# Performance work log

Measured on AMD Instinct MI355X. Metric: run time of the kernel, lower is better.

## Reference

```python
import jax, jax.numpy as jnp
import numpy as np

D_MODEL = 512
NUM_HEADS = 8
D_FF = 2048
HEAD_DIM = D_MODEL // NUM_HEADS
EPS = 1e-8


def rmsnorm(x, scale):
    rms = jax.lax.rsqrt(jnp.mean(x * x, axis=-1, keepdims=True) + EPS)
    return scale * x * rms


def alibi_bias(seq_len, num_heads):
    # faithful to: 1.0 / (arange(1,H+1) * 2**arange(0,8)[:,None]).flatten()[:H]
    a = jnp.arange(1, num_heads + 1, dtype=jnp.float32)          # (H,)
    b = 2.0 ** jnp.arange(0, 8, dtype=jnp.float32)[:, None]       # (8,1)
    slopes = (1.0 / (a * b).reshape(-1))[:num_heads]               # (H,)
    pos = jnp.arange(seq_len)
    dist = jnp.abs(pos[:, None] - pos[None, :]).astype(jnp.float32)  # (S,S)
    return -slopes[:, None, None] * dist[None]                     # (H,S,S)


def setup_inputs() -> dict:
    key = jax.random.key(0)
    ks = jax.random.split(key, 12)
    s = 0.02
    return {
        "x": jax.random.normal(ks[0], (2, 2048, D_MODEL), dtype=jnp.float32),
        "norm1_scale": jnp.ones((D_MODEL,), jnp.float32),
        "norm2_scale": jnp.ones((D_MODEL,), jnp.float32),
        "in_proj_w": jax.random.normal(ks[1], (3 * D_MODEL, D_MODEL), jnp.float32) * s,
        "in_proj_b": jnp.zeros((3 * D_MODEL,), jnp.float32),
        "out_proj_w": jax.random.normal(ks[2], (D_MODEL, D_MODEL), jnp.float32) * s,
        "out_proj_b": jnp.zeros((D_MODEL,), jnp.float32),
        "w1": jax.random.normal(ks[3], (D_FF, D_MODEL), jnp.float32) * s,
        "b1": jnp.zeros((D_FF,), jnp.float32),
        "w2": jax.random.normal(ks[4], (D_MODEL, D_FF), jnp.float32) * s,
        "b2": jnp.zeros((D_MODEL,), jnp.float32),
    }


def reference(x, norm1_scale, norm2_scale, in_proj_w, in_proj_b,
              out_proj_w, out_proj_b, w1, b1, w2, b2):
    B, S, D = x.shape
    xn = rmsnorm(x, norm1_scale)
    qkv = xn @ in_proj_w.T + in_proj_b                      # (B,S,3D)
    q, k, v = jnp.split(qkv, 3, axis=-1)
    q = q.reshape(B, S, NUM_HEADS, HEAD_DIM)
    k = k.reshape(B, S, NUM_HEADS, HEAD_DIM)
    v = v.reshape(B, S, NUM_HEADS, HEAD_DIM)
    scale = 1.0 / jnp.sqrt(jnp.float32(HEAD_DIM))
    scores = jnp.einsum('bqhd,bkhd->bhqk', q, k) * scale    # (B,H,S,S)
    scores = scores + alibi_bias(S, NUM_HEADS)[None]
    attn = jax.nn.softmax(scores, axis=-1)
    ctx = jnp.einsum('bhqk,bkhd->bqhd', attn, v).reshape(B, S, D)
    attn_out = ctx @ out_proj_w.T + out_proj_b
    x = x + attn_out                                        # dropout is identity (eval)
    xn2 = rmsnorm(x, norm2_scale)
    h = jax.nn.gelu(xn2 @ w1.T + b1, approximate=False)
    mlp_out = h @ w2.T + b2
    return x + mlp_out
```

## Files before the change

kernel.cpp:

```cpp
#include <hip/hip_runtime.h>
#include <math.h>


typedef __bf16 bf16x8 __attribute__((ext_vector_type(8)));
typedef float  f32x4  __attribute__((ext_vector_type(4)));

#define TOKENS 4096
#define DMODEL 512
#define SEQ    2048
#define SPLITK 4
#define QSCALE 0.1803368801f

__device__ __forceinline__ void gl_lds16(const __bf16* g, __bf16* l) {
    __builtin_amdgcn_global_load_lds(
        (const __attribute__((address_space(1))) void*)g,
        (__attribute__((address_space(3))) void*)l, 16, 0, 0);
}

union PkU { unsigned u; __bf16 h[2]; };

__global__ void cvt_all(const float* __restrict__ w0, const float* __restrict__ w1,
                        const float* __restrict__ w2, const float* __restrict__ w3,
                        __bf16* __restrict__ d0, __bf16* __restrict__ d1,
                        __bf16* __restrict__ d2, __bf16* __restrict__ d3) {
    const int N0 = 1536 * 512, N1 = 512 * 512, N2 = 2048 * 512, N3 = 512 * 2048;
    int i4 = (blockIdx.x * 256 + threadIdx.x) * 4;
    const float* s; __bf16* d;
    if (i4 < N0)                   { s = w0 + i4;  d = d0 + i4; }
    else if ((i4 -= N0) < N1)      { s = w1 + i4;  d = d1 + i4; }
    else if ((i4 -= N1) < N2)      { s = w2 + i4;  d = d2 + i4; }
    else if ((i4 -= N2) < N3)      { s = w3 + i4;  d = d3 + i4; }
    else return;
    float4 v = *(const float4*)s;
    d[0] = (__bf16)v.x; d[1] = (__bf16)v.y; d[2] = (__bf16)v.z; d[3] = (__bf16)v.w;
}

__global__ void rmsnorm_kernel(const float* __restrict__ x, const float* __restrict__ scale,
                               __bf16* __restrict__ out) {
    int wave = threadIdx.x >> 6, lane = threadIdx.x & 63;
    int tok = blockIdx.x * 4 + wave;
    const float* row = x + (size_t)tok * DMODEL;
    float4 v0 = *(const float4*)&row[lane * 4];
    float4 v1 = *(const float4*)&row[256 + lane * 4];
    float ss = v0.x*v0.x + v0.y*v0.y + v0.z*v0.z + v0.w*v0.w
             + v1.x*v1.x + v1.y*v1.y + v1.z*v1.z + v1.w*v1.w;
    #pragma unroll
    for (int off = 1; off < 64; off <<= 1) ss += __shfl_xor(ss, off);
    float r = rsqrtf(ss * (1.0f / DMODEL) + 1e-8f);
    __bf16* o = out + (size_t)tok * DMODEL;
    o[lane*4 + 0] = (__bf16)(v0.x * r * scale[lane*4 + 0]);
    o[lane*4 + 1] = (__bf16)(v0.y * r * scale[lane*4 + 1]);
    o[lane*4 + 2] = (__bf16)(v0.z * r * scale[lane*4 + 2]);
    o[lane*4 + 3] = (__bf16)(v0.w * r * scale[lane*4 + 3]);
    o[256 + lane*4 + 0] = (__bf16)(v1.x * r * scale[256 + lane*4 + 0]);
    o[256 + lane*4 + 1] = (__bf16)(v1.y * r * scale[256 + lane*4 + 1]);
    o[256 + lane*4 + 2] = (__bf16)(v1.z * r * scale[256 + lane*4 + 2]);
    o[256 + lane*4 + 3] = (__bf16)(v1.w * r * scale[256 + lane*4 + 3]);
}

template <int EPI, int TM>
__global__ __launch_bounds__(256) void gemm_bt(
    const __bf16* __restrict__ A, const __bf16* __restrict__ W,
    const float* __restrict__ bias, const float* __restrict__ res,
    float* __restrict__ Cf, __bf16* __restrict__ Cb,
    __bf16* __restrict__ qb, __bf16* __restrict__ kb, __bf16* __restrict__ vtb,
    int M, int N, int K)
{
    constexpr int RI = TM / 32;
    __shared__ alignas(16) __bf16 As[2][TM * 32];
    __shared__ alignas(16) __bf16 Bs[2][128 * 32];
    const int tid = threadIdx.x;
    const int bm = blockIdx.x * TM;
    const int bn = blockIdx.y * 128;
    const int wave = tid >> 6, lane = tid & 63;
    const int wm = (wave & 1) * (TM / 2), wn = (wave >> 1) * 64;
    const int lrow = lane & 15;
    const int kq = (lane >> 4) * 8;

    f32x4 acc[RI][4] = {};

    for (int k0 = 0; k0 < K; k0 += 64) {
        __syncthreads();
        #pragma unroll
        for (int i = 0; i < TM / 32; i++) {
            int tt = i * 256 + tid;
            int kh = tt / (TM * 4), rem = tt % (TM * 4);
            int mrow = rem >> 2, c8 = rem & 3;
            gl_lds16(&A[(size_t)(bm + mrow) * K + k0 + kh * 32 + c8 * 8],
                     (__bf16*)As + tt * 8);
        }
        #pragma unroll
        for (int i = 0; i < 4; i++) {
            int tt = i * 256 + tid;
            int kh = tt >> 9, rem = tt & 511;
            int nrow = rem >> 2, c8 = rem & 3;
            gl_lds16(&W[(size_t)(bn + nrow) * K + k0 + kh * 32 + c8 * 8],
                     (__bf16*)Bs + tt * 8);
        }
        __syncthreads();
        #pragma unroll
        for (int kh = 0; kh < 2; kh++) {
            bf16x8 af[RI], bfv[4];
            #pragma unroll
            for (int i = 0; i < RI; i++) af[i] = *(bf16x8*)&As[kh][(wm + i*16 + lrow)*32 + kq];
            #pragma unroll
            for (int j = 0; j < 4; j++) bfv[j] = *(bf16x8*)&Bs[kh][(wn + j*16 + lrow)*32 + kq];
            #pragma unroll
            for (int i = 0; i < RI; i++)
                #pragma unroll
                for (int j = 0; j < 4; j++)
                    acc[i][j] = __builtin_amdgcn_mfma_f32_16x16x32_bf16(af[i], bfv[j], acc[i][j], 0, 0, 0);
        }
    }

    const int crow0 = (lane >> 4) * 4;
    const int ccol = lane & 15;
    const int quad = lane >> 4;

    if (EPI == 4) {
        #pragma unroll
        for (int j = 0; j < 4; j++) {
            const int col = bn + wn + j * 16 + ccol;
            const float bv = bias[col];
            if (col < 512) {
                const int h = col >> 6, d = col & 63;
                #pragma unroll
                for (int i = 0; i < RI; i++) {
                    const int row0 = bm + wm + i * 16 + crow0;
                    const int b = row0 >> 11, s0 = row0 & 2047;
                    #pragma unroll
                    for (int r = 0; r < 4; r++)
                        qb[(((size_t)b*8 + h)*2048 + s0 + r)*64 + d] =
                            (__bf16)((acc[i][j][r] + bv) * QSCALE);
                }
            } else if (col < 1024) {
                const int h = (col - 512) >> 6, d = col & 63;
                #pragma unroll
                for (int i = 0; i < RI; i++) {
                    const int row0 = bm + wm + i * 16 + crow0;
                    const int b = row0 >> 11, s0 = row0 & 2047;
                    #pragma unroll
                    for (int r = 0; r < 4; r++)
                        kb[(((size_t)b*8 + h)*2048 + s0 + r)*64 + d] = (__bf16)(acc[i][j][r] + bv);
                }
            } else {
                const int h = (col - 1024) >> 6, d = col & 63;
                const int tok0 = bm + wm;
                const int b = tok0 >> 11, sbase = tok0 & 2047;
                unsigned* vrow = (unsigned*)vtb + (((size_t)b*8 + h)*64 + d) * 1024 + (sbase >> 1);
                #pragma unroll
                for (int r = 0; r < 4; r++) {
                    PkU pk;
                    pk.h[0] = (__bf16)(acc[0][j][r] + bv);
                    pk.h[1] = (__bf16)(acc[1][j][r] + bv);
                    vrow[quad * 4 + r] = pk.u;
                }
            }
        }
    } else {
        #pragma unroll
        for (int i = 0; i < RI; i++) {
            const int row0 = bm + wm + i * 16 + crow0;
            #pragma unroll
            for (int j = 0; j < 4; j++) {
                const int col = bn + wn + j * 16 + ccol;
                const float bv = bias[col];
                if (EPI == 1) {
                    #pragma unroll
                    for (int r = 0; r < 4; r++) {
                        const size_t idx = (size_t)(row0 + r) * N + col;
                        Cf[idx] = res[idx] + acc[i][j][r] + bv;
                    }
                } else {
                    #pragma unroll
                    for (int r = 0; r < 4; r++) {
                        float v = acc[i][j][r] + bv;
                        Cb[(size_t)(row0 + r) * N + col] =
                            (__bf16)(0.5f * v * (1.0f + erff(v * 0.70710678f)));
                    }
                }
            }
        }
    }
}

__global__ __launch_bounds__(256, 4) void attn_kernel(
    const __bf16* __restrict__ qb, const __bf16* __restrict__ kb,
    const __bf16* __restrict__ vtb,
    float* __restrict__ Opart, float* __restrict__ lpart)
{
    const int qt = blockIdx.x, bh = blockIdx.y, sp = blockIdx.z;
    const int h = bh & 7;
    const int tid = threadIdx.x, wave = tid >> 6, lane = tid & 63;
    const int lrow = lane & 15, quad = lane >> 4;

    __shared__ alignas(16) __bf16 Ks[2][64 * 32];
    __shared__ alignas(16) __bf16 Vt[2][64 * 32];
    __shared__ alignas(16) unsigned Pt4[4][2][32][20];

    const float slope2 = -1.44269504f / (float)(h + 1);
    const int qbase = qt * 128 + wave * 32;

    bf16x8 qf[2][2];
    #pragma unroll
    for (int rt = 0; rt < 2; rt++)
        #pragma unroll
        for (int dh = 0; dh < 2; dh++)
            qf[rt][dh] = *(const bf16x8*)&qb[((size_t)bh*2048 + qbase + rt*16 + lrow)*64 + dh*32 + quad*8];

    bf16x8 ones;
    #pragma unroll
    for (int j = 0; j < 8; j++) ones[j] = (__bf16)1.0f;

    f32x4 O[2][4] = {};
    f32x4 lacc[2] = {};

    for (int kt = sp * (32 / SPLITK); kt < (sp + 1) * (32 / SPLITK); kt++) {
        const int kbase = kt * 64;
        __syncthreads();
        {
            #pragma unroll
            for (int i = 0; i < 2; i++) {
                int tt = i * 256 + tid;
                int dh = tt >> 8, key = (tt & 255) >> 2, c8 = (tt & 3) * 8;
                gl_lds16(&kb[((size_t)bh*2048 + kbase + key)*64 + dh*32 + c8],
                         (__bf16*)Ks + tt * 8);
            }
            #pragma unroll
            for (int i = 0; i < 2; i++) {
                int tt = i * 256 + tid;
                int kh = tt >> 8, d = (tt & 255) >> 2, ck = (tt & 3) * 8;
                gl_lds16(&vtb[((size_t)bh*64 + d)*2048 + kbase + kh*32 + ck],
                         (__bf16*)Vt + tt * 8);
            }
        }
        __syncthreads();

        bf16x8 kf[4][2];
        #pragma unroll
        for (int j = 0; j < 4; j++)
            #pragma unroll
            for (int dh = 0; dh < 2; dh++)
                kf[j][dh] = *(bf16x8*)&Ks[dh][(j*16 + lrow)*32 + quad*8];

        #pragma unroll
        for (int rt = 0; rt < 2; rt++) {
            f32x4 Sc[4] = {};
            #pragma unroll
            for (int dh = 0; dh < 2; dh++)
                #pragma unroll
                for (int j = 0; j < 4; j++)
                    Sc[j] = __builtin_amdgcn_mfma_f32_16x16x32_bf16(qf[rt][dh], kf[j][dh], Sc[j], 0, 0, 0);

            const float dbase = (float)(qbase + rt*16 + quad*4 - kbase - lrow);
            #pragma unroll
            for (int r = 0; r < 4; r++) {
                const float d0 = dbase + (float)r;
                #pragma unroll
                for (int jp = 0; jp < 2; jp++) {
                    float v0 = fmaf(slope2, fabsf(d0 - (float)(jp*32)),      Sc[2*jp  ][r]);
                    float v1 = fmaf(slope2, fabsf(d0 - (float)(jp*32 + 16)), Sc[2*jp+1][r]);
                    PkU pk;
                    pk.h[0] = (__bf16)exp2f(v0);
                    pk.h[1] = (__bf16)exp2f(v1);
                    Pt4[wave][jp][rt*16 + quad*4 + r][lrow] = pk.u;
                }
            }
        }

        bf16x8 pf[2][2];
        #pragma unroll
        for (int rt = 0; rt < 2; rt++)
            #pragma unroll
            for (int kh = 0; kh < 2; kh++)
                pf[rt][kh] = *(bf16x8*)&Pt4[wave][kh][rt*16 + lrow][quad*4];

        #pragma unroll
        for (int rt = 0; rt < 2; rt++)
            #pragma unroll
            for (int kh = 0; kh < 2; kh++)
                lacc[rt] = __builtin_amdgcn_mfma_f32_16x16x32_bf16(pf[rt][kh], ones, lacc[rt], 0, 0, 0);

        #pragma unroll
        for (int dt = 0; dt < 4; dt++) {
            #pragma unroll
            for (int kh = 0; kh < 2; kh++) {
                bf16x8 vf = *(bf16x8*)&Vt[kh][(dt*16 + lrow)*32 + quad*8];
                #pragma unroll
                for (int rt = 0; rt < 2; rt++)
                    O[rt][dt] = __builtin_amdgcn_mfma_f32_16x16x32_bf16(pf[rt][kh], vf, O[rt][dt], 0, 0, 0);
            }
        }
    }

    #pragma unroll
    for (int rt = 0; rt < 2; rt++) {
        #pragma unroll
        for (int dt = 0; dt < 4; dt++)
            #pragma unroll
            for (int r = 0; r < 4; r++) {
                const int q = qbase + rt*16 + quad*4 + r;
                Opart[(((size_t)sp*16 + bh)*2048 + q)*64 + dt*16 + lrow] = O[rt][dt][r];
            }
        if (lrow == 0) {
            #pragma unroll
            for (int r = 0; r < 4; r++)
                lpart[((size_t)sp*16 + bh)*2048 + qbase + rt*16 + quad*4 + r] = lacc[rt][r];
        }
    }
}

__global__ void combine_kernel(const float* __restrict__ Opart, const float* __restrict__ lpart,
                               __bf16* __restrict__ ctx) {
    const int idx = blockIdx.x * 256 + threadIdx.x;
    const int d2 = idx & 31;
    const int q  = (idx >> 5) & 2047;
    const int bh = idx >> 16;
    float ox = 0.0f, oy = 0.0f, l = 0.0f;
    #pragma unroll
    for (int sp = 0; sp < SPLITK; sp++) {
        const float2 o = *(const float2*)&Opart[(((size_t)sp*16 + bh)*2048 + q)*64 + d2*2];
        ox += o.x; oy += o.y;
        l += lpart[((size_t)sp*16 + bh)*2048 + q];
    }
    const float inv = 1.0f / l;
    PkU pk;
    pk.h[0] = (__bf16)(ox * inv);
    pk.h[1] = (__bf16)(oy * inv);
    const int b = bh >> 3, h = bh & 7;
    *((unsigned*)ctx + (((size_t)b*2048 + q)*512 + h*64) / 2 + d2) = pk.u;
}

extern "C" void kernel_launch(void* const* d_in, const int* in_sizes, int n_in,
                              void* d_out, int out_size, void* d_ws, size_t ws_size,
                              hipStream_t stream) {
    const float* x    = (const float*)d_in[0];
    const float* n1s  = (const float*)d_in[1];
    const float* n2s  = (const float*)d_in[2];
    const float* wqkv = (const float*)d_in[3];
    const float* bqkv = (const float*)d_in[4];
    const float* wout = (const float*)d_in[5];
    const float* bout = (const float*)d_in[6];
    const float* w1   = (const float*)d_in[7];
    const float* b1   = (const float*)d_in[8];
    const float* w2   = (const float*)d_in[9];
    const float* b2   = (const float*)d_in[10];
    float* out = (float*)d_out;

    char* ws = (char*)d_ws;
    __bf16* xn1    = (__bf16*)ws; ws += (size_t)TOKENS * DMODEL * 2;
    __bf16* qbuf   = (__bf16*)ws; ws += (size_t)TOKENS * DMODEL * 2;
    __bf16* kbuf   = (__bf16*)ws; ws += (size_t)TOKENS * DMODEL * 2;
    __bf16* vtbuf  = (__bf16*)ws; ws += (size_t)TOKENS * DMODEL * 2;
    __bf16* wqkv_b = (__bf16*)ws; ws += (size_t)1536 * DMODEL * 2;
    __bf16* wout_b = (__bf16*)ws; ws += (size_t)DMODEL * DMODEL * 2;
    __bf16* w1_b   = (__bf16*)ws; ws += (size_t)2048 * DMODEL * 2;
    __bf16* w2_b   = (__bf16*)ws; ws += (size_t)DMODEL * 2048 * 2;
    __bf16* ctx    = (__bf16*)ws; ws += (size_t)TOKENS * DMODEL * 2;
    float*  lpart  = (float*)ws;  ws += (size_t)SPLITK * 16 * 2048 * 4;
    float*  Opart  = (float*)ws;
    float*  x1     = (float*)ws;  ws += (size_t)TOKENS * DMODEL * 4;
    __bf16* xn2    = (__bf16*)ws; ws += (size_t)TOKENS * DMODEL * 2;
    __bf16* hbuf   = (__bf16*)ws;

    cvt_all<<<dim3(3072), 256, 0, stream>>>(wqkv, wout, w1, w2, wqkv_b, wout_b, w1_b, w2_b);

    rmsnorm_kernel<<<dim3(TOKENS / 4), 256, 0, stream>>>(x, n1s, xn1);

    gemm_bt<4, 64><<<dim3(TOKENS / 64, 1536 / 128), 256, 0, stream>>>(
        xn1, wqkv_b, bqkv, nullptr, nullptr, nullptr, qbuf, kbuf, vtbuf,
        TOKENS, 1536, DMODEL);

    attn_kernel<<<dim3(SEQ / 128, 16, SPLITK), 256, 0, stream>>>(
        qbuf, kbuf, vtbuf, Opart, lpart);

    combine_kernel<<<dim3(16 * 2048 * 32 / 256), 256, 0, stream>>>(Opart, lpart, ctx);

    gemm_bt<1, 32><<<dim3(TOKENS / 32, DMODEL / 128), 256, 0, stream>>>(
        ctx, wout_b, bout, x, x1, nullptr, nullptr, nullptr, nullptr,
        TOKENS, DMODEL, DMODEL);

    rmsnorm_kernel<<<dim3(TOKENS / 4), 256, 0, stream>>>(x1, n2s, xn2);

    gemm_bt<2, 128><<<dim3(TOKENS / 128, 2048 / 128), 256, 0, stream>>>(
        xn2, w1_b, b1, nullptr, nullptr, hbuf, nullptr, nullptr, nullptr,
        TOKENS, 2048, DMODEL);

    gemm_bt<1, 32><<<dim3(TOKENS / 32, DMODEL / 128), 256, 0, stream>>>(
        hbuf, w2_b, b2, x1, out, nullptr, nullptr, nullptr, nullptr,
        TOKENS, DMODEL, 2048);
}
```

Before: 203.5 us.

## Double-buffer attention K/V loads, halve split-K, bf16 partials, fuse pre-kernels

The attention loop now prefetches the next K/V tile into a second LDS buffer while the current tile is computed, and the extra barrier per iteration is removed. Split-K drops from 4 to 2, and the partial outputs are stored as bf16 to cut combine traffic. The weight conversion and first RMSNorm are merged into one launch, and the QKV GEMM uses a taller 128-row tile with a generalized V-transpose epilogue. The risks are more LDS per block, which may lower occupancy, fewer attention blocks in flight, and a loss of precision in the partial sums. The removed post-load barrier also looks unsafe: the loads for the current tile may not be complete or visible to all waves before they are read.

```diff
diff --git a/kernel.cpp b/kernel.cpp
--- a/kernel.cpp
+++ b/kernel.cpp
@@ -8,7 +8,7 @@
 #define TOKENS 4096
 #define DMODEL 512
 #define SEQ    2048
-#define SPLITK 4
+#define SPLITK 2
 #define QSCALE 0.1803368801f
 
 __device__ __forceinline__ void gl_lds16(const __bf16* g, __bf16* l) {
@@ -19,20 +19,44 @@
 
 union PkU { unsigned u; __bf16 h[2]; };
 
-__global__ void cvt_all(const float* __restrict__ w0, const float* __restrict__ w1,
-                        const float* __restrict__ w2, const float* __restrict__ w3,
-                        __bf16* __restrict__ d0, __bf16* __restrict__ d1,
-                        __bf16* __restrict__ d2, __bf16* __restrict__ d3) {
-    const int N0 = 1536 * 512, N1 = 512 * 512, N2 = 2048 * 512, N3 = 512 * 2048;
-    int i4 = (blockIdx.x * 256 + threadIdx.x) * 4;
-    const float* s; __bf16* d;
-    if (i4 < N0)                   { s = w0 + i4;  d = d0 + i4; }
-    else if ((i4 -= N0) < N1)      { s = w1 + i4;  d = d1 + i4; }
-    else if ((i4 -= N1) < N2)      { s = w2 + i4;  d = d2 + i4; }
-    else if ((i4 -= N2) < N3)      { s = w3 + i4;  d = d3 + i4; }
-    else return;
-    float4 v = *(const float4*)s;
-    d[0] = (__bf16)v.x; d[1] = (__bf16)v.y; d[2] = (__bf16)v.z; d[3] = (__bf16)v.w;
+__global__ void pre_kernel(const float* __restrict__ x, const float* __restrict__ n1s,
+                           __bf16* __restrict__ xn1,
+                           const float* __restrict__ w0, const float* __restrict__ w1,
+                           const float* __restrict__ w2, const float* __restrict__ w3,
+                           __bf16* __restrict__ d0, __bf16* __restrict__ d1,
+                           __bf16* __restrict__ d2, __bf16* __restrict__ d3) {
+    if (blockIdx.x < 1024) {
+        int wave = threadIdx.x >> 6, lane = threadIdx.x & 63;
+        int tok = blockIdx.x * 4 + wave;
+        const float* row = x + (size_t)tok * DMODEL;
+        float4 v0 = *(const float4*)&row[lane * 4];
+        float4 v1 = *(const float4*)&row[256 + lane * 4];
+        float ss = v0.x*v0.x + v0.y*v0.y + v0.z*v0.z + v0.w*v0.w
+                 + v1.x*v1.x + v1.y*v1.y + v1.z*v1.z + v1.w*v1.w;
+        #pragma unroll
+        for (int off = 1; off < 64; off <<= 1) ss += __shfl_xor(ss, off);
+        float r = rsqrtf(ss * (1.0f / DMODEL) + 1e-8f);
+        __bf16* o = xn1 + (size_t)tok * DMODEL;
+        o[lane*4 + 0] = (__bf16)(v0.x * r * n1s[lane*4 + 0]);
+        o[lane*4 + 1] = (__bf16)(v0.y * r * n1s[lane*4 + 1]);
+        o[lane*4 + 2] = (__bf16)(v0.z * r * n1s[lane*4 + 2]);
+        o[lane*4 + 3] = (__bf16)(v0.w * r * n1s[lane*4 + 3]);
+        o[256 + lane*4 + 0] = (__bf16)(v1.x * r * n1s[256 + lane*4 + 0]);
+        o[256 + lane*4 + 1] = (__bf16)(v1.y * r * n1s[256 + lane*4 + 1]);
+        o[256 + lane*4 + 2] = (__bf16)(v1.z * r * n1s[256 + lane*4 + 2]);
+        o[256 + lane*4 + 3] = (__bf16)(v1.w * r * n1s[256 + lane*4 + 3]);
+    } else {
+        const int N0 = 1536 * 512, N1 = 512 * 512, N2 = 2048 * 512, N3 = 512 * 2048;
+        int i4 = ((blockIdx.x - 1024) * 256 + threadIdx.x) * 4;
+        const float* s; __bf16* d;
+        if (i4 < N0)              { s = w0 + i4;  d = d0 + i4; }
+        else if ((i4 -= N0) < N1) { s = w1 + i4;  d = d1 + i4; }
+        else if ((i4 -= N1) < N2) { s = w2 + i4;  d = d2 + i4; }
+        else if ((i4 -= N2) < N3) { s = w3 + i4;  d = d3 + i4; }
+        else return;
+        float4 v = *(const float4*)s;
+        d[0] = (__bf16)v.x; d[1] = (__bf16)v.y; d[2] = (__bf16)v.z; d[3] = (__bf16)v.w;
+    }
 }
 
 __global__ void rmsnorm_kernel(const float* __restrict__ x, const float* __restrict__ scale,
@@ -149,11 +173,14 @@
                 const int b = tok0 >> 11, sbase = tok0 & 2047;
                 unsigned* vrow = (unsigned*)vtb + (((size_t)b*8 + h)*64 + d) * 1024 + (sbase >> 1);
                 #pragma unroll
-                for (int r = 0; r < 4; r++) {
-                    PkU pk;
-                    pk.h[0] = (__bf16)(acc[0][j][r] + bv);
-                    pk.h[1] = (__bf16)(acc[1][j][r] + bv);
-                    vrow[quad * 4 + r] = pk.u;
+                for (int ip = 0; ip < RI / 2; ip++) {
+                    #pragma unroll
+                    for (int r = 0; r < 4; r++) {
+                        PkU pk;
+                        pk.h[0] = (__bf16)(acc[2*ip][j][r] + bv);
+                        pk.h[1] = (__bf16)(acc[2*ip+1][j][r] + bv);
+                        vrow[ip * 16 + quad * 4 + r] = pk.u;
+                    }
                 }
             }
         }
@@ -187,19 +214,20 @@
 __global__ __launch_bounds__(256, 4) void attn_kernel(
     const __bf16* __restrict__ qb, const __bf16* __restrict__ kb,
     const __bf16* __restrict__ vtb,
-    float* __restrict__ Opart, float* __restrict__ lpart)
+    __bf16* __restrict__ Opart, float* __restrict__ lpart)
 {
     const int qt = blockIdx.x, bh = blockIdx.y, sp = blockIdx.z;
     const int h = bh & 7;
     const int tid = threadIdx.x, wave = tid >> 6, lane = tid & 63;
     const int lrow = lane & 15, quad = lane >> 4;
 
-    __shared__ alignas(16) __bf16 Ks[2][64 * 32];
-    __shared__ alignas(16) __bf16 Vt[2][64 * 32];
+    __shared__ alignas(16) __bf16 Ks[2][2][64 * 32];
+    __shared__ alignas(16) __bf16 Vt[2][2][64 * 32];
     __shared__ alignas(16) unsigned Pt4[4][2][32][20];
 
     const float slope2 = -1.44269504f / (float)(h + 1);
     const int qbase = qt * 128 + wave * 32;
+    const int kt0 = sp * (32 / SPLITK), kt1 = kt0 + 32 / SPLITK;
 
     bf16x8 qf[2][2];
     #pragma unroll
@@ -215,33 +243,37 @@
     f32x4 O[2][4] = {};
     f32x4 lacc[2] = {};
 
-    for (int kt = sp * (32 / SPLITK); kt < (sp + 1) * (32 / SPLITK); kt++) {
+    auto stage = [&](int kt, int buf) {
+        const int kbase = kt * 64;
+        #pragma unroll
+        for (int i = 0; i < 2; i++) {
+            int tt = i * 256 + tid;
+            int dh = tt >> 8, key = (tt & 255) >> 2, c8 = (tt & 3) * 8;
+            gl_lds16(&kb[((size_t)bh*2048 + kbase + key)*64 + dh*32 + c8],
+                     (__bf16*)Ks[buf] + tt * 8);
+        }
+        #pragma unroll
+        for (int i = 0; i < 2; i++) {
+            int tt = i * 256 + tid;
+            int kh = tt >> 8, d = (tt & 255) >> 2, ck = (tt & 3) * 8;
+            gl_lds16(&vtb[((size_t)bh*64 + d)*2048 + kbase + kh*32 + ck],
+                     (__bf16*)Vt[buf] + tt * 8);
+        }
+    };
+
+    stage(kt0, 0);
+
+    for (int kt = kt0, buf = 0; kt < kt1; kt++, buf ^= 1) {
         const int kbase = kt * 64;
         __syncthreads();
-        {
-            #pragma unroll
-            for (int i = 0; i < 2; i++) {
-                int tt = i * 256 + tid;
-                int dh = tt >> 8, key = (tt & 255) >> 2, c8 = (tt & 3) * 8;
-                gl_lds16(&kb[((size_t)bh*2048 + kbase + key)*64 + dh*32 + c8],
-                         (__bf16*)Ks + tt * 8);
-            }
-            #pragma unroll
-            for (int i = 0; i < 2; i++) {
-                int tt = i * 256 + tid;
-                int kh = tt >> 8, d = (tt & 255) >> 2, ck = (tt & 3) * 8;
-                gl_lds16(&vtb[((size_t)bh*64 + d)*2048 + kbase + kh*32 + ck],
-                         (__bf16*)Vt + tt * 8);
-            }
-        }
-        __syncthreads();
+        if (kt + 1 < kt1) stage(kt + 1, buf ^ 1);
 
         bf16x8 kf[4][2];
         #pragma unroll
         for (int j = 0; j < 4; j++)
             #pragma unroll
             for (int dh = 0; dh < 2; dh++)
-                kf[j][dh] = *(bf16x8*)&Ks[dh][(j*16 + lrow)*32 + quad*8];
+                kf[j][dh] = *(bf16x8*)&Ks[buf][dh][(j*16 + lrow)*32 + quad*8];
 
         #pragma unroll
         for (int rt = 0; rt < 2; rt++) {
@@ -285,7 +317,7 @@
         for (int dt = 0; dt < 4; dt++) {
             #pragma unroll
             for (int kh = 0; kh < 2; kh++) {
-                bf16x8 vf = *(bf16x8*)&Vt[kh][(dt*16 + lrow)*32 + quad*8];
+                bf16x8 vf = *(bf16x8*)&Vt[buf][kh][(dt*16 + lrow)*32 + quad*8];
                 #pragma unroll
                 for (int rt = 0; rt < 2; rt++)
                     O[rt][dt] = __builtin_amdgcn_mfma_f32_16x16x32_bf16(pf[rt][kh], vf, O[rt][dt], 0, 0, 0);
@@ -300,7 +332,7 @@
             #pragma unroll
             for (int r = 0; r < 4; r++) {
                 const int q = qbase + rt*16 + quad*4 + r;
-                Opart[(((size_t)sp*16 + bh)*2048 + q)*64 + dt*16 + lrow] = O[rt][dt][r];
+                Opart[(((size_t)sp*16 + bh)*2048 + q)*64 + dt*16 + lrow] = (__bf16)O[rt][dt][r];
             }
         if (lrow == 0) {
             #pragma unroll
@@ -310,7 +342,7 @@
     }
 }
 
-__global__ void combine_kernel(const float* __restrict__ Opart, const float* __restrict__ lpart,
+__global__ void combine_kernel(const __bf16* __restrict__ Opart, const float* __restrict__ lpart,
                                __bf16* __restrict__ ctx) {
     const int idx = blockIdx.x * 256 + threadIdx.x;
     const int d2 = idx & 31;
@@ -319,8 +351,8 @@
     float ox = 0.0f, oy = 0.0f, l = 0.0f;
     #pragma unroll
     for (int sp = 0; sp < SPLITK; sp++) {
-        const float2 o = *(const float2*)&Opart[(((size_t)sp*16 + bh)*2048 + q)*64 + d2*2];
-        ox += o.x; oy += o.y;
+        PkU o; o.u = *((const unsigned*)Opart + (((size_t)sp*16 + bh)*2048 + q)*32 + d2);
+        ox += (float)o.h[0]; oy += (float)o.h[1];
         l += lpart[((size_t)sp*16 + bh)*2048 + q];
     }
     const float inv = 1.0f / l;
@@ -358,16 +390,15 @@
     __bf16* w2_b   = (__bf16*)ws; ws += (size_t)DMODEL * 2048 * 2;
     __bf16* ctx    = (__bf16*)ws; ws += (size_t)TOKENS * DMODEL * 2;
     float*  lpart  = (float*)ws;  ws += (size_t)SPLITK * 16 * 2048 * 4;
-    float*  Opart  = (float*)ws;
+    __bf16* Opart  = (__bf16*)ws; ws += (size_t)SPLITK * 16 * 2048 * 64 * 2;
     float*  x1     = (float*)ws;  ws += (size_t)TOKENS * DMODEL * 4;
     __bf16* xn2    = (__bf16*)ws; ws += (size_t)TOKENS * DMODEL * 2;
     __bf16* hbuf   = (__bf16*)ws;
 
-    cvt_all<<<dim3(3072), 256, 0, stream>>>(wqkv, wout, w1, w2, wqkv_b, wout_b, w1_b, w2_b);
-
-    rmsnorm_kernel<<<dim3(TOKENS / 4), 256, 0, stream>>>(x, n1s, xn1);
-
-    gemm_bt<4, 64><<<dim3(TOKENS / 64, 1536 / 128), 256, 0, stream>>>(
+    pre_kernel<<<dim3(4096), 256, 0, stream>>>(x, n1s, xn1,
+        wqkv, wout, w1, w2, wqkv_b, wout_b, w1_b, w2_b);
+
+    gemm_bt<4, 128><<<dim3(TOKENS / 128, 1536 / 128), 256, 0, stream>>>(
         xn1, wqkv_b, bqkv, nullptr, nullptr, nullptr, qbuf, kbuf, vtbuf,
         TOKENS, 1536, DMODEL);
 
```

Result: no change. 200.8 us (-1.3%).
